# Performance work log

Measured on AMD Instinct MI355X. Metric: run time of the kernel, lower is better.

Reference implementation:

```python
import jax, jax.numpy as jnp
import numpy as np

K_F = 3
NUM = K_F * K_F - 1      # 8 non-reference neighbors
IDX_REF = NUM // 2       # 4: reference pixel inserted in the middle
PROP_TIME = 18


def _conv2d(x, w, b, pad):
    y = jax.lax.conv_general_dilated(x, w, (1, 1), [(pad, pad), (pad, pad)],
                                     dimension_numbers=("NCHW", "OIHW", "NCHW"))
    return y + b[None, :, None, None]


def _offset_affinity(guidance, conv_w, conv_b, aff_scale):
    # TGASS branch of _get_offset_affinity
    B, _, H, W = guidance.shape
    pad_g = (conv_w.shape[2] - 1) // 2
    oa = _conv2d(guidance, conv_w, conv_b, pad_g)          # [B, 3*NUM, H, W]
    o1, o2, aff = jnp.split(oa, 3, axis=1)
    # torch: cat((o1,o2),1).view(B, NUM, 2, H, W) -- plain reinterpret of channels
    off = jnp.concatenate([o1, o2], axis=1).reshape(B, NUM, 2, H, W)
    zeros = jnp.zeros((B, 1, 2, H, W), off.dtype)
    off = jnp.concatenate([off[:, :IDX_REF], zeros, off[:, IDX_REF:]], axis=1)  # [B,9,2,H,W]
    aff = jnp.tanh(aff) / (aff_scale + 1e-8)               # TGASS scaling
    s = jnp.sum(jnp.abs(aff), axis=1, keepdims=True) + 1e-4
    s = jnp.maximum(s, 1.0)                                # aff_abs_sum[<1]=1
    aff = aff / s
    aff_ref = 1.0 - jnp.sum(aff, axis=1, keepdims=True)
    aff = jnp.concatenate([aff[:, :IDX_REF], aff_ref, aff[:, IDX_REF:]], axis=1)  # [B,9,H,W]
    return off.reshape(B, 2 * (NUM + 1), H, W), aff


def _bilinear(img, y, x):
    # img [B,H,W]; y,x [B,K,H,W] absolute sampling coords; zero outside (DCN zero padding)
    H, W = img.shape[1], img.shape[2]
    y0 = jnp.floor(y)
    x0 = jnp.floor(x)
    ty = y - y0
    tx = x - x0

    def g(yi, xi):
        valid = (yi >= 0) & (yi <= H - 1) & (xi >= 0) & (xi <= W - 1)
        yc = jnp.clip(yi, 0, H - 1).astype(jnp.int32)
        xc = jnp.clip(xi, 0, W - 1).astype(jnp.int32)
        v = jax.vmap(lambda im, a, b: im[a, b])(img, yc, xc)
        return jnp.where(valid, v, 0.0)

    return ((1 - ty) * (1 - tx) * g(y0, x0) + (1 - ty) * tx * g(y0, x0 + 1)
            + ty * (1 - tx) * g(y0 + 1, x0) + ty * tx * g(y0 + 1, x0 + 1))


def _nlspn_forward(feat_init, guidance, confidence, conv_w, conv_b, aff_scale):
    B, _, H, W = feat_init.shape
    dt = feat_init.dtype
    offset, aff = _offset_affinity(guidance, conv_w, conv_b, aff_scale)
    off = offset.reshape(B, NUM + 1, 2, H, W)
    off_y, off_x = off[:, :, 0], off[:, :, 1]              # [B,9,H,W]
    kk = jnp.arange(NUM + 1)
    grid_y = (kk // K_F - 1).astype(dt)[None, :, None, None]
    grid_x = (kk % K_F - 1).astype(dt)[None, :, None, None]
    base_y = jnp.arange(H, dtype=dt)[None, None, :, None]
    base_x = jnp.arange(W, dtype=dt)[None, None, None, :]
    # absolute sampling coordinates, constant across propagation steps
    yy = base_y + grid_y + off_y                           # [B,9,H,W]
    xx = base_x + grid_x + off_x

    def step(feat, _):
        # modulated deform conv with w==1, b==0, groups=1: weighted gather-sum
        s = _bilinear((feat * confidence)[:, 0], yy, xx)   # [B,9,H,W]
        nf = jnp.sum(aff * s, axis=1, keepdims=True)       # [B,1,H,W]
        return nf, nf

    feat_final, feats = jax.lax.scan(step, feat_init, None, length=PROP_TIME)
    return feat_final, feats, offset, aff, aff_scale


def setup_inputs() -> dict:
    key = jax.random.key(0)
    k1, k2, k3, k4 = jax.random.split(key, 4)
    B, CG, H, W = 4, 8, 240, 1216
    feat_init = jax.random.uniform(k1, (B, 1, H, W), dtype=jnp.float32)
    guidance = jax.random.normal(k2, (B, CG, H, W), dtype=jnp.float32)
    confidence = jax.random.uniform(k3, (B, 1, H, W), dtype=jnp.float32)
    conv_w = 0.1 * jax.random.normal(k4, (3 * NUM, CG, 3, 3), dtype=jnp.float32)
    conv_b = jnp.zeros((3 * NUM,), jnp.float32)
    aff_scale = jnp.full((1,), 0.5 * NUM, jnp.float32)     # affinity_gamma * num
    return {"feat_init": feat_init, "guidance": guidance, "confidence": confidence,
            "conv_w": conv_w, "conv_b": conv_b, "aff_scale": aff_scale}


def reference(feat_init, guidance, confidence, conv_w, conv_b, aff_scale):
    return _nlspn_forward(feat_init, guidance, confidence, conv_w, conv_b, aff_scale)
```

## Files before the change

### kernel.cpp

```cpp
#include <hip/hip_runtime.h>

#define BB 4
#define CG 8
#define HH 240
#define WW 1216
#define HW (HH*WW)
#define NPIX (BB*HW)

#define TW 128
#define TH 4
#define MG 8
#define LW (TW + 2*MG)
#define LH (TH + 2*MG)
#define NXT ((WW + TW - 1)/TW)
#define NYT (HH/TH)

__global__ __launch_bounds__(256) void conv_fused(
    const float* __restrict__ g, const float* __restrict__ cw,
    const float* __restrict__ cb, const float* __restrict__ asc,
    const float* __restrict__ feat_init, const float* __restrict__ conf,
    float* __restrict__ out_off, float* __restrict__ out_aff,
    float* __restrict__ out_scale,
    unsigned long long* __restrict__ paf, float* __restrict__ tav,
    float* __restrict__ fc0)
{
    int gid = blockIdx.x * 256 + threadIdx.x;
    if (gid == 0) out_scale[0] = asc[0];
    if (gid >= NPIX) return;
    int w = gid % WW;
    int tmp = gid / WW;
    int h = tmp % HH;
    int b = tmp / HH;

    const float* gb = g + (size_t)b * CG * HW;

    float gvals[9 * CG];
    #pragma unroll
    for (int kh = 0; kh < 3; ++kh) {
        int y = h + kh - 1;
        float my = ((unsigned)y < (unsigned)HH) ? 1.0f : 0.0f;
        int yc = min(max(y, 0), HH - 1);
        #pragma unroll
        for (int kw = 0; kw < 3; ++kw) {
            int x = w + kw - 1;
            float m = ((unsigned)x < (unsigned)WW) ? my : 0.0f;
            int xc = min(max(x, 0), WW - 1);
            const float* p = gb + yc * WW + xc;
            #pragma unroll
            for (int ch = 0; ch < CG; ++ch)
                gvals[ch * 9 + kh * 3 + kw] = m * p[(size_t)ch * HW];
        }
    }

    float acc[24];
    #pragma unroll
    for (int o = 0; o < 24; ++o) acc[o] = cb[o];

    #pragma unroll
    for (int ch = 0; ch < CG; ++ch) {
        #pragma unroll
        for (int kh = 0; kh < 3; ++kh) {
            #pragma unroll
            for (int kw = 0; kw < 3; ++kw) {
                float xv = gvals[ch * 9 + kh * 3 + kw];
                #pragma unroll
                for (int o = 0; o < 24; ++o)
                    acc[o] = fmaf(xv, cw[((o * CG + ch) * 3 + kh) * 3 + kw], acc[o]);
            }
        }
    }

    int pix = h * WW + w;

    float oyk[9], oxk[9];
    #pragma unroll
    for (int k = 0; k < 9; ++k) {
        if (k < 4)       { oyk[k] = acc[2 * k];     oxk[k] = acc[2 * k + 1]; }
        else if (k == 4) { oyk[k] = 0.0f;           oxk[k] = 0.0f; }
        else             { oyk[k] = acc[2 * k - 2]; oxk[k] = acc[2 * k - 1]; }
        __builtin_nontemporal_store(oyk[k], &out_off[(size_t)(b * 18 + 2 * k) * HW + pix]);
        __builtin_nontemporal_store(oxk[k], &out_off[(size_t)(b * 18 + 2 * k + 1) * HW + pix]);
    }

    float inv = 1.0f / (asc[0] + 1e-8f);
    float a[8];
    float s = 0.0f;
    #pragma unroll
    for (int c = 0; c < 8; ++c) {
        a[c] = tanhf(acc[16 + c]) * inv;
        s += fabsf(a[c]);
    }
    s += 1e-4f;
    s = fmaxf(s, 1.0f);
    float sum = 0.0f;
    #pragma unroll
    for (int c = 0; c < 8; ++c) {
        a[c] = a[c] / s;
        sum += a[c];
    }
    float a9[9];
    #pragma unroll
    for (int c = 0; c < 4; ++c) a9[c] = a[c];
    a9[4] = 1.0f - sum;
    #pragma unroll
    for (int c = 4; c < 8; ++c) a9[c + 1] = a[c];

    #pragma unroll
    for (int k = 0; k < 9; ++k)
        __builtin_nontemporal_store(a9[k], &out_aff[(size_t)(b * 9 + k) * HW + pix]);

    if (paf) {
        #pragma unroll
        for (int k = 0; k < 9; ++k) {
            tav[(size_t)k * NPIX + gid] = a9[k];
            if (k == 4) continue;
            int j = (k < 4) ? k : k - 1;

            float yy = (float)(h + k / 3 - 1) + oyk[k];
            float xx = (float)(w + k % 3 - 1) + oxk[k];
            float y0f = floorf(yy), x0f = floorf(xx);
            float tyf = yy - y0f, txf = xx - x0f;

            unsigned vy0 = (y0f >= 0.0f   && y0f <= 239.0f)  ? 1u : 0u;
            unsigned vy1 = (y0f >= -1.0f  && y0f <= 238.0f)  ? 1u : 0u;
            unsigned vx0 = (x0f >= 0.0f   && x0f <= 1215.0f) ? 1u : 0u;
            unsigned vx1 = (x0f >= -1.0f  && x0f <= 1214.0f) ? 1u : 0u;

            int y0i = (int)fminf(fmaxf(y0f, -1.0f), 239.0f);
            int x0i = (int)fminf(fmaxf(x0f, -1.0f), 1215.0f);

            unsigned pack = (unsigned)(y0i + 1) | ((unsigned)(x0i + 1) << 8)
                          | (vy0 << 19) | (vy1 << 20) | (vx0 << 21) | (vx1 << 22);
            unsigned tyq = (unsigned)(fminf(tyf, 0.99999f) * 65535.0f + 0.5f);
            unsigned txq = (unsigned)(fminf(txf, 0.99999f) * 65535.0f + 0.5f);
            unsigned frac = tyq | (txq << 16);

            paf[(size_t)j * NPIX + gid] =
                (unsigned long long)pack | ((unsigned long long)frac << 32);
        }
        fc0[gid] = feat_init[gid] * conf[gid];
    }
}

__global__ __launch_bounds__(512) void prop4(
    const float* __restrict__ fcIn, const float* __restrict__ conf,
    const unsigned long long* __restrict__ paf, const float* __restrict__ tav,
    float* __restrict__ fout, float* __restrict__ fcOut, float* __restrict__ ffinal)
{
    __shared__ float sfc[LH * LW];

    int bx = blockIdx.x % NXT;
    int by = blockIdx.x / NXT;
    int b  = blockIdx.y;
    int xs = bx * TW, ys = by * TH;

    int rlo = max(0, ys - MG), rhi = min(HH - 1, ys + TH - 1 + MG);
    int clo = max(0, xs - MG), chi = min(WW - 1, xs + TW - 1 + MG);
    int rh = rhi - rlo + 1;

    const float* fcb = fcIn + (size_t)b * HW;

    for (int i = threadIdx.x; i < rh * LW; i += 512) {
        int r = i / LW;
        int c = i - r * LW;
        int col = min(clo + c, WW - 1);
        sfc[i] = fcb[(rlo + r) * WW + col];
    }
    __syncthreads();

    int tx = threadIdx.x & (TW - 1);
    int tyy = threadIdx.x >> 7;
    int x = xs + tx, y = ys + tyy;
    if (x >= WW) return;
    int pix = y * WW + x;
    int gid = b * HW + pix;

    float res = tav[(size_t)4 * NPIX + gid] *
                sfc[(y - rlo) * LW + (x - clo)];

    #pragma unroll
    for (int j = 0; j < 8; ++j) {
        int k = (j < 4) ? j : j + 1;
        unsigned long long pf = paf[(size_t)j * NPIX + gid];
        float av = tav[(size_t)k * NPIX + gid];

        unsigned Px = (unsigned)pf;
        unsigned Py = (unsigned)(pf >> 32);

        int y0 = (int)(Px & 0xffu) - 1;
        int x0 = (int)((Px >> 8) & 0x7ffu) - 1;
        float ty = (float)(Py & 0xffffu) * (1.0f / 65535.0f);
        float txf = (float)(Py >> 16)    * (1.0f / 65535.0f);
        float fy0 = (Px & (1u << 19)) ? 1.0f : 0.0f;
        float fy1 = (Px & (1u << 20)) ? 1.0f : 0.0f;
        float fx0 = (Px & (1u << 21)) ? 1.0f : 0.0f;
        float fx1 = (Px & (1u << 22)) ? 1.0f : 0.0f;

        int yA = max(y0, 0), yB = min(y0 + 1, HH - 1);
        int xA = max(x0, 0), xB = min(x0 + 1, WW - 1);

        float v00, v01, v10, v11;
        if (yA >= rlo && yB <= rhi && xA >= clo && xB <= chi) {
            int rA = (yA - rlo) * LW - clo;
            int rB = (yB - rlo) * LW - clo;
            v00 = sfc[rA + xA]; v01 = sfc[rA + xB];
            v10 = sfc[rB + xA]; v11 = sfc[rB + xB];
        } else {
            int rA = yA * WW, rB = yB * WW;
            v00 = fcb[rA + xA]; v01 = fcb[rA + xB];
            v10 = fcb[rB + xA]; v11 = fcb[rB + xB];
        }

        float cy0 = fy0 * (1.0f - ty),  cy1 = fy1 * ty;
        float cx0 = fx0 * (1.0f - txf), cx1 = fx1 * txf;

        float u0 = fmaf(cx1, v01, cx0 * v00);
        float u1 = fmaf(cx1, v11, cx0 * v10);
        res = fmaf(av, fmaf(cy1, u1, cy0 * u0), res);
    }
    __builtin_nontemporal_store(res, &fout[gid]);
    if (fcOut)  fcOut[gid] = res * conf[gid];
    if (ffinal) __builtin_nontemporal_store(res, &ffinal[gid]);
}

__device__ __forceinline__ float sampPC(const float* __restrict__ fb,
                                        const float* __restrict__ cf,
                                        int y, int x) {
    bool valid = ((unsigned)y < (unsigned)HH) && ((unsigned)x < (unsigned)WW);
    int yc = min(max(y, 0), HH - 1);
    int xc = min(max(x, 0), WW - 1);
    int idx = yc * WW + xc;
    float v = fb[idx] * cf[idx];
    return valid ? v : 0.0f;
}

__global__ __launch_bounds__(256) void prop(
    const float* __restrict__ fp, const float* __restrict__ conf,
    const float* __restrict__ off, const float* __restrict__ aff,
    float* __restrict__ fout, float* __restrict__ ffinal)
{
    int gid = blockIdx.x * 256 + threadIdx.x;
    if (gid >= NPIX) return;
    int w = gid % WW;
    int tmp = gid / WW;
    int h = tmp % HH;
    int b = tmp / HH;
    int pix = h * WW + w;

    const float* fb = fp + (size_t)b * HW;
    const float* cf = conf + (size_t)b * HW;

    float res = 0.0f;
    #pragma unroll
    for (int k = 0; k < 9; ++k) {
        float oy = off[(size_t)(b * 18 + 2 * k) * HW + pix];
        float ox = off[(size_t)(b * 18 + 2 * k + 1) * HW + pix];
        float av = aff[(size_t)(b * 9 + k) * HW + pix];

        float yy = (float)(h + k / 3 - 1) + oy;
        float xx = (float)(w + k % 3 - 1) + ox;

        float y0f = floorf(yy), x0f = floorf(xx);
        float ty = yy - y0f, tx = xx - x0f;
        int y0 = (int)y0f, x0 = (int)x0f;

        float v00 = sampPC(fb, cf, y0,     x0);
        float v01 = sampPC(fb, cf, y0,     x0 + 1);
        float v10 = sampPC(fb, cf, y0 + 1, x0);
        float v11 = sampPC(fb, cf, y0 + 1, x0 + 1);

        float sk = (1.0f - ty) * (1.0f - tx) * v00
                 + (1.0f - ty) * tx          * v01
                 + ty          * (1.0f - tx) * v10
                 + ty          * tx          * v11;
        res = fmaf(av, sk, res);
    }
    fout[gid] = res;
    if (ffinal) ffinal[gid] = res;
}

extern "C" void kernel_launch(void* const* d_in, const int* in_sizes, int n_in,
                              void* d_out, int out_size, void* d_ws, size_t ws_size,
                              hipStream_t stream) {
    const float* feat_init  = (const float*)d_in[0];
    const float* guidance   = (const float*)d_in[1];
    const float* confidence = (const float*)d_in[2];
    const float* conv_w     = (const float*)d_in[3];
    const float* conv_b     = (const float*)d_in[4];
    const float* aff_scale  = (const float*)d_in[5];

    float* out        = (float*)d_out;
    float* feat_final = out;
    float* feats      = out + (size_t)NPIX;
    float* offset     = out + (size_t)19 * NPIX;
    float* affout     = out + (size_t)37 * NPIX;
    float* scale_out  = out + (size_t)46 * NPIX;

    int nblocks = (NPIX + 255) / 256;

    size_t need = (size_t)8 * NPIX * 8 + (size_t)9 * NPIX * 4 + (size_t)2 * NPIX * 4;

    if (ws_size >= need) {
        char* wsb = (char*)d_ws;
        unsigned long long* paf = (unsigned long long*)wsb;
        float* tav = (float*)(wsb + (size_t)8 * NPIX * 8);
        float* fcA = (float*)(wsb + (size_t)8 * NPIX * 8 + (size_t)9 * NPIX * 4);
        float* fcB = fcA + NPIX;

        conv_fused<<<nblocks, 256, 0, stream>>>(guidance, conv_w, conv_b, aff_scale,
                                                feat_init, confidence,
                                                offset, affout, scale_out,
                                                paf, tav, fcA);

        dim3 pgrid(NXT * NYT, BB);
        float* fcIn = fcA;
        float* fcOut = fcB;
        for (int t = 0; t < 18; ++t) {
            float* cur = feats + (size_t)t * NPIX;
            prop4<<<pgrid, 512, 0, stream>>>(fcIn, confidence, paf, tav, cur,
                                             (t == 17) ? nullptr : fcOut,
                                             (t == 17) ? feat_final : nullptr);
            float* tmpp = fcIn; fcIn = fcOut; fcOut = tmpp;
        }
    } else {
        conv_fused<<<nblocks, 256, 0, stream>>>(guidance, conv_w, conv_b, aff_scale,
                                                feat_init, confidence,
                                                offset, affout, scale_out,
                                                nullptr, nullptr, nullptr);
        const float* prev = feat_init;
        for (int t = 0; t < 18; ++t) {
            float* cur = feats + (size_t)t * NPIX;
            prop<<<nblocks, 256, 0, stream>>>(prev, confidence, offset, affout, cur,
                                              (t == 17) ? feat_final : nullptr);
            prev = cur;
        }
    }
}
```

Measured before the change: 652.0 us.

## Drop duplicate affinity buffer, read output affinity in propagation, tile conv blocks 2D

The conv kernel stops writing a separate per-k affinity workspace (tav), and the propagation kernel now reads affinities straight from the output affinity tensor using nontemporal loads. The packed offset loads are also made nontemporal. The conv kernel switches to a 2D tiled grid of 64x4 pixels with a fast interior path that skips the bounds clamping and masking. The aim is to cut the 9-plane workspace write and reduce address arithmetic. The risk is that nontemporal loads could bypass caching for data that is reread on every one of the 18 iterations.

```diff
diff --git a/kernel.cpp b/kernel.cpp
--- a/kernel.cpp
+++ b/kernel.cpp
@@ -15,40 +15,58 @@
 #define NXT ((WW + TW - 1)/TW)
 #define NYT (HH/TH)
 
+#define CBX 19
+#define CBY 60
+
 __global__ __launch_bounds__(256) void conv_fused(
     const float* __restrict__ g, const float* __restrict__ cw,
     const float* __restrict__ cb, const float* __restrict__ asc,
     const float* __restrict__ feat_init, const float* __restrict__ conf,
     float* __restrict__ out_off, float* __restrict__ out_aff,
     float* __restrict__ out_scale,
-    unsigned long long* __restrict__ paf, float* __restrict__ tav,
-    float* __restrict__ fc0)
+    unsigned long long* __restrict__ paf, float* __restrict__ fc0)
 {
-    int gid = blockIdx.x * 256 + threadIdx.x;
-    if (gid == 0) out_scale[0] = asc[0];
-    if (gid >= NPIX) return;
-    int w = gid % WW;
-    int tmp = gid / WW;
-    int h = tmp % HH;
-    int b = tmp / HH;
+    int bx = blockIdx.x % CBX;
+    int by = blockIdx.x / CBX;
+    int b  = blockIdx.y;
+    if (blockIdx.x == 0 && b == 0 && threadIdx.x == 0) out_scale[0] = asc[0];
+
+    int tx = threadIdx.x & 63;
+    int ty = threadIdx.x >> 6;
+    int w = bx * 64 + tx;
+    int h = by * 4 + ty;
+    int pix = h * WW + w;
+    int gid = b * HW + pix;
 
     const float* gb = g + (size_t)b * CG * HW;
 
     float gvals[9 * CG];
-    #pragma unroll
-    for (int kh = 0; kh < 3; ++kh) {
-        int y = h + kh - 1;
-        float my = ((unsigned)y < (unsigned)HH) ? 1.0f : 0.0f;
-        int yc = min(max(y, 0), HH - 1);
+    bool interior = (bx > 0) & (bx < CBX - 1) & (by > 0) & (by < CBY - 1);
+    if (interior) {
+        const float* p = gb + (h - 1) * WW + (w - 1);
         #pragma unroll
-        for (int kw = 0; kw < 3; ++kw) {
-            int x = w + kw - 1;
-            float m = ((unsigned)x < (unsigned)WW) ? my : 0.0f;
-            int xc = min(max(x, 0), WW - 1);
-            const float* p = gb + yc * WW + xc;
+        for (int ch = 0; ch < CG; ++ch)
             #pragma unroll
-            for (int ch = 0; ch < CG; ++ch)
-                gvals[ch * 9 + kh * 3 + kw] = m * p[(size_t)ch * HW];
+            for (int kh = 0; kh < 3; ++kh)
+                #pragma unroll
+                for (int kw = 0; kw < 3; ++kw)
+                    gvals[ch * 9 + kh * 3 + kw] = p[(size_t)ch * HW + kh * WW + kw];
+    } else {
+        #pragma unroll
+        for (int kh = 0; kh < 3; ++kh) {
+            int y = h + kh - 1;
+            float my = ((unsigned)y < (unsigned)HH) ? 1.0f : 0.0f;
+            int yc = min(max(y, 0), HH - 1);
+            #pragma unroll
+            for (int kw = 0; kw < 3; ++kw) {
+                int x = w + kw - 1;
+                float m = ((unsigned)x < (unsigned)WW) ? my : 0.0f;
+                int xc = min(max(x, 0), WW - 1);
+                const float* p = gb + yc * WW + xc;
+                #pragma unroll
+                for (int ch = 0; ch < CG; ++ch)
+                    gvals[ch * 9 + kh * 3 + kw] = m * p[(size_t)ch * HW];
+            }
         }
     }
 
@@ -70,8 +88,6 @@
         }
     }
 
-    int pix = h * WW + w;
-
     float oyk[9], oxk[9];
     #pragma unroll
     for (int k = 0; k < 9; ++k) {
@@ -112,7 +128,6 @@
     if (paf) {
         #pragma unroll
         for (int k = 0; k < 9; ++k) {
-            tav[(size_t)k * NPIX + gid] = a9[k];
             if (k == 4) continue;
             int j = (k < 4) ? k : k - 1;
 
@@ -144,7 +159,7 @@
 
 __global__ __launch_bounds__(512) void prop4(
     const float* __restrict__ fcIn, const float* __restrict__ conf,
-    const unsigned long long* __restrict__ paf, const float* __restrict__ tav,
+    const unsigned long long* __restrict__ paf, const float* __restrict__ affq,
     float* __restrict__ fout, float* __restrict__ fcOut, float* __restrict__ ffinal)
 {
     __shared__ float sfc[LH * LW];
@@ -175,14 +190,14 @@
     int pix = y * WW + x;
     int gid = b * HW + pix;
 
-    float res = tav[(size_t)4 * NPIX + gid] *
+    float res = __builtin_nontemporal_load(&affq[(size_t)(b * 9 + 4) * HW + pix]) *
                 sfc[(y - rlo) * LW + (x - clo)];
 
     #pragma unroll
     for (int j = 0; j < 8; ++j) {
         int k = (j < 4) ? j : j + 1;
-        unsigned long long pf = paf[(size_t)j * NPIX + gid];
-        float av = tav[(size_t)k * NPIX + gid];
+        unsigned long long pf = __builtin_nontemporal_load(&paf[(size_t)j * NPIX + gid]);
+        float av = __builtin_nontemporal_load(&affq[(size_t)(b * 9 + k) * HW + pix]);
 
         unsigned Px = (unsigned)pf;
         unsigned Py = (unsigned)(pf >> 32);
@@ -296,38 +311,38 @@
     float* affout     = out + (size_t)37 * NPIX;
     float* scale_out  = out + (size_t)46 * NPIX;
 
-    int nblocks = (NPIX + 255) / 256;
-
-    size_t need = (size_t)8 * NPIX * 8 + (size_t)9 * NPIX * 4 + (size_t)2 * NPIX * 4;
+    size_t need = (size_t)8 * NPIX * 8 + (size_t)2 * NPIX * 4;
+
+    dim3 cgrid(CBX * CBY, BB);
 
     if (ws_size >= need) {
         char* wsb = (char*)d_ws;
         unsigned long long* paf = (unsigned long long*)wsb;
-        float* tav = (float*)(wsb + (size_t)8 * NPIX * 8);
-        float* fcA = (float*)(wsb + (size_t)8 * NPIX * 8 + (size_t)9 * NPIX * 4);
+        float* fcA = (float*)(wsb + (size_t)8 * NPIX * 8);
         float* fcB = fcA + NPIX;
 
-        conv_fused<<<nblocks, 256, 0, stream>>>(guidance, conv_w, conv_b, aff_scale,
-                                                feat_init, confidence,
-                                                offset, affout, scale_out,
-                                                paf, tav, fcA);
+        conv_fused<<<cgrid, 256, 0, stream>>>(guidance, conv_w, conv_b, aff_scale,
+                                              feat_init, confidence,
+                                              offset, affout, scale_out,
+                                              paf, fcA);
 
         dim3 pgrid(NXT * NYT, BB);
         float* fcIn = fcA;
         float* fcOut = fcB;
         for (int t = 0; t < 18; ++t) {
             float* cur = feats + (size_t)t * NPIX;
-            prop4<<<pgrid, 512, 0, stream>>>(fcIn, confidence, paf, tav, cur,
+            prop4<<<pgrid, 512, 0, stream>>>(fcIn, confidence, paf, affout, cur,
                                              (t == 17) ? nullptr : fcOut,
                                              (t == 17) ? feat_final : nullptr);
             float* tmpp = fcIn; fcIn = fcOut; fcOut = tmpp;
         }
     } else {
-        conv_fused<<<nblocks, 256, 0, stream>>>(guidance, conv_w, conv_b, aff_scale,
-                                                feat_init, confidence,
-                                                offset, affout, scale_out,
-                                                nullptr, nullptr, nullptr);
+        conv_fused<<<cgrid, 256, 0, stream>>>(guidance, conv_w, conv_b, aff_scale,
+                                              feat_init, confidence,
+                                              offset, affout, scale_out,
+                                              nullptr, nullptr);
         const float* prev = feat_init;
+        int nblocks = (NPIX + 255) / 256;
         for (int t = 0; t < 18; ++t) {
             float* cur = feats + (size_t)t * NPIX;
             prop<<<nblocks, 256, 0, stream>>>(prev, confidence, offset, affout, cur,
```

After: 798.5 us. 1.22x slower.
